# Kernel optimization log

Hardware: AMD Instinct MI355X
Metric: run time of the kernel (lower is better)

The kernel has to match this reference:

```python
import jax, jax.numpy as jnp
import numpy as np

B, N, E, H = 256, 256, 256, 512


def setup_inputs() -> dict:
    key = jax.random.key(0)
    ks = jax.random.split(key, 8)
    sH = 1.0 / np.sqrt(H)  # torch default init scale for LSTMCell / Linear fan_in
    sE = 1.0 / np.sqrt(E)
    return {
        "encoder_output": jax.random.normal(ks[0], (B, N, E), dtype=jnp.float32),
        "W_ih": jax.random.uniform(ks[1], (4 * H, E), jnp.float32, -sH, sH),
        "W_hh": jax.random.uniform(ks[2], (4 * H, H), jnp.float32, -sH, sH),
        "b_ih": jax.random.uniform(ks[3], (4 * H,), jnp.float32, -sH, sH),
        "b_hh": jax.random.uniform(ks[4], (4 * H,), jnp.float32, -sH, sH),
        "W_q": jax.random.uniform(ks[5], (H, H), jnp.float32, -sH, sH),
        "W_k": jax.random.uniform(ks[6], (H, E), jnp.float32, -sE, sE),
        "v": jax.random.uniform(ks[7], (H,), jnp.float32, -sH, sH),
        "max_steps": 256,
    }


def reference(encoder_output, W_ih, W_hh, b_ih, b_hh, W_q, W_k, v, max_steps):
    b, n, e = encoder_output.shape
    h_dim = W_hh.shape[1]
    # W_k(encoder_output) is loop-invariant -> hoist (same math as original)
    k_enc = jnp.einsum("bne,he->bnh", encoder_output, W_k)  # (B, N, H)
    keys = jax.random.split(jax.random.key(42), max_steps)
    batch_idx = jnp.arange(b)

    def step(carry, key):
        h, c, start, visited_mask = carry
        # torch LSTMCell: gates in i, f, g, o order
        gates = start @ W_ih.T + b_ih + h @ W_hh.T + b_hh  # (B, 4H)
        i, f, g, o = jnp.split(gates, 4, axis=-1)
        c = jax.nn.sigmoid(f) * c + jax.nn.sigmoid(i) * jnp.tanh(g)
        h = jax.nn.sigmoid(o) * jnp.tanh(c)
        q = h @ W_q.T  # (B, H)
        scores = jnp.einsum("bnh,h->bn", jnp.tanh(q[:, None, :] + k_enc), v)
        scores = scores - 1.0e6 * visited_mask
        probs = jax.nn.softmax(scores, axis=-1)
        # multinomial(probs, 1) == categorical over masked scores (logits)
        idx = jax.random.categorical(key, scores)  # (B,) int
        action_prob = jnp.take_along_axis(probs, idx[:, None], axis=1)[:, 0]
        visited_mask = visited_mask.at[batch_idx, idx].set(1.0)
        start = encoder_output[batch_idx, idx]  # (B, E)
        return (h, c, start, visited_mask), (idx, action_prob)

    init = (
        jnp.zeros((b, h_dim), jnp.float32),
        jnp.zeros((b, h_dim), jnp.float32),
        jnp.zeros((b, e), jnp.float32),
        jnp.zeros((b, n), jnp.float32),
    )
    _, (seq, action_probs) = jax.lax.scan(step, init, keys)
    action_sequence = seq.T  # (B, max_steps)
    logp_sum = jnp.sum(action_probs, axis=0)  # (B,) -- sums probs, as original does
    return action_sequence, logp_sum
```

## Files before the change

### kernel.cpp

```cpp
#include <hip/hip_runtime.h>
#include <cstdint>
#include <math.h>

typedef unsigned int u32;

#define BB 256
#define NN 256
#define EE 256
#define HH 512
#define G4 2048
#define KK 768
#define TT 256
#define NBLK 256
#define NTHR 1024

#define ALOADD(p)    __hip_atomic_load((p), __ATOMIC_RELAXED, __HIP_MEMORY_SCOPE_AGENT)
#define ASTORED(p,v) __hip_atomic_store((p), (v), __ATOMIC_RELAXED, __HIP_MEMORY_SCOPE_AGENT)
#define ALOADI(p)    __hip_atomic_load((p), __ATOMIC_RELAXED, __HIP_MEMORY_SCOPE_AGENT)
#define ASTOREI(p,v) __hip_atomic_store((p), (v), __ATOMIC_RELAXED, __HIP_MEMORY_SCOPE_AGENT)

__device__ __forceinline__ u32 rotl(u32 x, int d) { return (x << d) | (x >> (32 - d)); }

__device__ __forceinline__ void tf4(u32& x0, u32& x1, int r0, int r1, int r2, int r3) {
  x0 += x1; x1 = rotl(x1, r0); x1 ^= x0;
  x0 += x1; x1 = rotl(x1, r1); x1 ^= x0;
  x0 += x1; x1 = rotl(x1, r2); x1 ^= x0;
  x0 += x1; x1 = rotl(x1, r3); x1 ^= x0;
}

__device__ __forceinline__ void threefry2x32(u32 k0, u32 k1, u32 x0, u32 x1, u32& o0, u32& o1) {
  u32 k2 = k0 ^ k1 ^ 0x1BD11BDAu;
  x0 += k0; x1 += k1;
  tf4(x0, x1, 13, 15, 26, 6);  x0 += k1; x1 += k2 + 1u;
  tf4(x0, x1, 17, 29, 16, 24); x0 += k2; x1 += k0 + 2u;
  tf4(x0, x1, 13, 15, 26, 6);  x0 += k0; x1 += k1 + 3u;
  tf4(x0, x1, 17, 29, 16, 24); x0 += k1; x1 += k2 + 4u;
  tf4(x0, x1, 13, 15, 26, 6);  x0 += k2; x1 += k0 + 5u;
  o0 = x0; o1 = x1;
}

struct Args {
  const float *enc, *W_ih, *W_hh, *b_ih, *b_hh, *W_q, *W_k, *v;
  float *out;
  float *kT;
  float *Wc;
  float *WqT;
  double *bsum;
  u32 *keys;
  double *h0, *h1;
  double *c;
  double *q;
  int *idx;
  u32 *flags;
};

__device__ __forceinline__ void grid_barrier(u32* cnt, u32* gen) {
  __syncthreads();
  if (threadIdx.x == 0) {
    u32 g = __hip_atomic_load(gen, __ATOMIC_RELAXED, __HIP_MEMORY_SCOPE_AGENT);
    __threadfence();
    if (atomicAdd(cnt, 1u) == NBLK - 1u) {
      __hip_atomic_store(cnt, 0u, __ATOMIC_RELAXED, __HIP_MEMORY_SCOPE_AGENT);
      __threadfence();
      atomicAdd(gen, 1u);
    } else {
      while (__hip_atomic_load(gen, __ATOMIC_RELAXED, __HIP_MEMORY_SCOPE_AGENT) == g) {
        __builtin_amdgcn_s_sleep(2);
      }
    }
    __threadfence();
  }
  __syncthreads();
}

__device__ __forceinline__ void pod_signal(u32* ph, int pod, int me, u32 val) {
  asm volatile("s_waitcnt vmcnt(0)" ::: "memory");
  __syncthreads();
  if (threadIdx.x == 0) ASTOREI(&ph[pod * 32 + me], val);
}
__device__ __forceinline__ void pod_wait(u32* ph, int pod, u32 target) {
  const int t = threadIdx.x;
  if (t < 32) {
    while (ALOADI(&ph[pod * 32 + t]) < target) { __builtin_amdgcn_s_sleep(1); }
  }
  __syncthreads();
}

__global__ __launch_bounds__(NTHR) void mono_kernel(Args a) {
  const int blk = blockIdx.x;
  const int t = threadIdx.x;
  __shared__ alignas(16) unsigned char SMRAW[42368];
  __shared__ int visS[NN];
  __shared__ float vSp[HH];
  __shared__ double logpS;
  const int grp = blk >> 5;
  const int me  = blk & 31;
  const int jb = 4 * (blk & 7) + ((blk >> 3) & 3);
  u32* p1f = a.flags;
  u32* qf  = a.flags + 256;
  u32* p2f = a.flags + 512;

  {
    const int tid = blk * NTHR + t;
    const int tot = NBLK * NTHR;
    if (tid < BB * HH) { a.h0[tid] = 0.0; a.c[tid] = 0.0; }
    if (tid < BB) a.idx[tid] = -1;
    if (tid < 256) {
      u32 o0, o1;
      threefry2x32(0u, 42u, 0u, (u32)tid, o0, o1);
      a.keys[2 * tid] = o0; a.keys[2 * tid + 1] = o1;
    }
    if (tid < G4) a.bsum[tid] = (double)a.b_ih[tid] + (double)a.b_hh[tid];
    for (int i = tid; i < HH * HH; i += tot) {
      int h2 = i >> 9, h = i & 511;
      a.WqT[i] = a.W_q[h * HH + h2];
    }
    for (int i = tid; i < KK * G4; i += tot) {
      int k = i >> 11, col = i & 2047;
      int x16 = col >> 6, g = (col >> 4) & 3, w = col & 15;
      int j = g * HH + x16 * 16 + w;
      a.Wc[i] = (k < EE) ? a.W_ih[j * EE + k] : a.W_hh[j * HH + (k - EE)];
    }
    if (t < NN) visS[t] = 0;
    if (t < HH) vSp[t] = a.v[t];
    if (t == 0) logpS = 0.0;
  }
  {
    float (*encS)[65] = (float(*)[65])SMRAW;
    float (*wkS)[65]  = (float(*)[65])(SMRAW + 64 * 65 * 4);
    const int tn = t & 63, th = t >> 6;
    for (int tile = blk; tile < 8 * 4 * BB; tile += NBLK) {
      const int bx = tile & 7, by = (tile >> 3) & 3, b = tile >> 5;
      const int h0i = bx * 64, n0 = by * 64;
      double acc[4];
#pragma unroll
      for (int i = 0; i < 4; i++) acc[i] = 0.0;
      for (int ec = 0; ec < EE; ec += 64) {
        __syncthreads();
#pragma unroll
        for (int i = 0; i < 4; i++) {
          int idx = i * NTHR + t; int r = idx >> 6, cc = idx & 63;
          encS[r][cc] = a.enc[((size_t)b * NN + n0 + r) * EE + ec + cc];
          wkS[r][cc]  = a.W_k[(size_t)(h0i + r) * EE + ec + cc];
        }
        __syncthreads();
#pragma unroll 8
        for (int e = 0; e < 64; e++) {
          double ev = (double)encS[tn][e];
#pragma unroll
          for (int i = 0; i < 4; i++) acc[i] += (double)wkS[th * 4 + i][e] * ev;
        }
      }
#pragma unroll
      for (int i = 0; i < 4; i++)
        a.kT[((size_t)b * HH + h0i + th * 4 + i) * NN + n0 + tn] = (float)acc[i];
    }
  }
  grid_barrier(a.flags + 768, a.flags + 800);

  for (int step = 0; step < TT; step++) {
    double* hPrev = (step & 1) ? a.h1 : a.h0;
    double* hCur  = (step & 1) ? a.h0 : a.h1;
    const int b0 = grp * 32;

    if (step > 0) pod_wait(p2f, grp, (u32)step);

    {
      double (*aS)[33] = (double(*)[33])SMRAW;
      double (*bS)[66] = (double(*)[66])(SMRAW + 8448);
      int* idxP = (int*)(SMRAW + 25344);
      const int sr = t >> 5, scp = t & 31;
      const int bk = t >> 6, bc = t & 63;
      if (t < 32) idxP[t] = ALOADI(&a.idx[b0 + t]);
      __syncthreads();

      double aR; float bR0, bR1;
      {
        int iv = idxP[sr];
        aR = (iv >= 0) ? (double)a.enc[((size_t)(b0 + sr) * NN + iv) * EE + scp] : 0.0;
        bR0 = a.Wc[(size_t)(bk)      * G4 + jb * 64 + bc];
        bR1 = a.Wc[(size_t)(bk + 16) * G4 + jb * 64 + bc];
      }
      const int jc = t & 63, rg2 = t >> 6;
      double acc0, acc1, acc2, acc3;
      {
        double bv = a.bsum[(jc >> 4) * HH + jb * 16 + (jc & 15)];
        acc0 = bv; acc1 = bv; acc2 = bv; acc3 = bv;
      }
      for (int kc = 0; kc < KK; kc += 32) {
        aS[sr][scp] = aR;
        bS[bk][bc]      = (double)bR0;
        bS[bk + 16][bc] = (double)bR1;
        int kn = kc + 32;
        if (kn < KK) {
          if (kn < EE) {
            int iv = idxP[sr];
            aR = (iv >= 0) ? (double)a.enc[((size_t)(b0 + sr) * NN + iv) * EE + kn + scp] : 0.0;
          } else {
            aR = ALOADD(&hPrev[(size_t)(b0 + sr) * HH + (kn - EE) + scp]);
          }
          bR0 = a.Wc[(size_t)(kn + bk)      * G4 + jb * 64 + bc];
          bR1 = a.Wc[(size_t)(kn + bk + 16) * G4 + jb * 64 + bc];
        }
        __syncthreads();
        if (t < 512) {
#pragma unroll 8
          for (int kk = 0; kk < 32; kk++) {
            double bv = bS[kk][jc];
            acc0 += aS[rg2 * 4][kk]     * bv;
            acc1 += aS[rg2 * 4 + 1][kk] * bv;
            acc2 += aS[rg2 * 4 + 2][kk] * bv;
            acc3 += aS[rg2 * 4 + 3][kk] * bv;
          }
        }
        __syncthreads();
      }
      double (*gS)[66] = (double(*)[66])SMRAW;
      if (t < 512) {
        gS[rg2 * 4][jc]     = acc0;
        gS[rg2 * 4 + 1][jc] = acc1;
        gS[rg2 * 4 + 2][jc] = acc2;
        gS[rg2 * 4 + 3][jc] = acc3;
      }
      __syncthreads();
      if (t < 512) {
        const int b = t >> 4, w = t & 15;
        double ig = gS[b][w], fg = gS[b][16 + w], gv = gS[b][32 + w], og = gS[b][48 + w];
        double si = 1.0 / (1.0 + exp(-ig));
        double sf = 1.0 / (1.0 + exp(-fg));
        double so = 1.0 / (1.0 + exp(-og));
        size_t ci = (size_t)(b0 + b) * HH + jb * 16 + w;
        double cn = sf * a.c[ci] + si * tanh(gv);
        a.c[ci] = cn;
        ASTORED(&hCur[ci], so * tanh(cn));
      }
    }
    pod_signal(p1f, grp, me, (u32)(step + 1));
    pod_wait(p1f, grp, (u32)(step + 1));

    {
      double (*hS)[33] = (double(*)[33])SMRAW;
      float  (*wS)[17] = (float (*)[17])(SMRAW + 8448);
      const int sr = t >> 5, scp = t & 31;
      const int wk = t >> 4, wj = t & 15;
      const int j0 = jb * 16;
      double hR = ALOADD(&hCur[(size_t)(b0 + sr) * HH + scp]);
      float  wR = (t < 512) ? a.WqT[(size_t)wk * HH + j0 + wj] : 0.0f;
      const int bq = t >> 4, j = t & 15;
      double p0 = 0.0, p1 = 0.0, p2 = 0.0, p3 = 0.0;
      for (int kc = 0; kc < HH; kc += 32) {
        hS[sr][scp] = hR;
        if (t < 512) wS[wk][wj] = wR;
        int kn = kc + 32;
        if (kn < HH) {
          hR = ALOADD(&hCur[(size_t)(b0 + sr) * HH + kn + scp]);
          if (t < 512) wR = a.WqT[(size_t)(kn + wk) * HH + j0 + wj];
        }
        __syncthreads();
        if (t < 512) {
#pragma unroll 8
          for (int kk = 0; kk < 32; kk += 4) {
            p0 += hS[bq][kk]     * (double)wS[kk][j];
            p1 += hS[bq][kk + 1] * (double)wS[kk + 1][j];
            p2 += hS[bq][kk + 2] * (double)wS[kk + 2][j];
            p3 += hS[bq][kk + 3] * (double)wS[kk + 3][j];
          }
        }
        __syncthreads();
      }
      if (t < 512)
        ASTORED(&a.q[(size_t)(b0 + bq) * HH + j0 + j], (p0 + p1) + (p2 + p3));
    }
    pod_signal(qf, grp, me, (u32)(step + 1));
    pod_wait(qf, grp, (u32)(step + 1));

    {
      double* qS  = (double*)SMRAW;
      double* pS  = (double*)(SMRAW + 4096);
      double* sS  = (double*)(SMRAW + 37120);
      double* red = (double*)(SMRAW + 39168);
      int*   redi = (int*)(SMRAW + 41216);
      int*   idxS = (int*)(SMRAW + 42240);
      const int b = blk;
      if (t < 512) qS[t] = ALOADD(&a.q[(size_t)b * HH + t]);
      __syncthreads();

      const int col4 = (t & 63) * 4, slice = t >> 6;
      const float* kp = a.kT + ((size_t)b * HH + slice * 32) * NN + col4;
      double c0 = 0.0, c1 = 0.0, c2 = 0.0, c3 = 0.0;
#pragma unroll 4
      for (int h = 0; h < 32; h++) {
        float4 kv = *(const float4*)(kp + (size_t)h * NN);
        int hh = slice * 32 + h;
        double qh = qS[hh];
        double vh = (double)vSp[hh];
        c0 += vh * (double)tanhf((float)(qh + (double)kv.x));
        c1 += vh * (double)tanhf((float)(qh + (double)kv.y));
        c2 += vh * (double)tanhf((float)(qh + (double)kv.z));
        c3 += vh * (double)tanhf((float)(qh + (double)kv.w));
      }
      {
        double* pw = pS + slice * 258 + col4;
        pw[0] = c0; pw[1] = c1; pw[2] = c2; pw[3] = c3;
      }
      __syncthreads();

      if (t < 256) {
        double s = 0.0;
#pragma unroll
        for (int sl = 0; sl < 16; sl++) s += pS[sl * 258 + t];
        if (visS[t]) s -= 1.0e6;
        sS[t] = s;
      }
      __syncthreads();

      if (t < 256) {
        u32 fl = (u32)(b * 256 + t);
        u32 o0, o1;
        threefry2x32(a.keys[2 * step], a.keys[2 * step + 1], 0u, fl, o0, o1);
        u32 bits = o0 ^ o1;
        u32 fb = (bits >> 9) | 0x3F800000u;
        float uf = __uint_as_float(fb) - 1.0f;
        double uu = (uf > 0.0f) ? (double)uf : (double)1.17549435e-38f;
        double gmb = -log(-log(uu));
        red[t] = gmb + sS[t];
        redi[t] = t;
      }
      __syncthreads();
      for (int s2 = 128; s2 > 0; s2 >>= 1) {
        if (t < s2) {
          double v1 = red[t], v2 = red[t + s2];
          int i1 = redi[t], i2 = redi[t + s2];
          if (v2 > v1 || (v2 == v1 && i2 < i1)) { red[t] = v2; redi[t] = i2; }
        }
        __syncthreads();
      }
      if (t == 0) *idxS = redi[0];
      __syncthreads();

      if (t == 0) {
        int bi = *idxS;
        visS[bi] = 1;
        ASTOREI(&a.idx[b], bi);
      }
      pod_signal(p2f, grp, me, (u32)(step + 1));

      if (t < 256) red[t] = sS[t];
      __syncthreads();
      for (int s2 = 128; s2 > 0; s2 >>= 1) {
        if (t < s2) red[t] = fmax(red[t], red[t + s2]);
        __syncthreads();
      }
      double m = red[0];
      __syncthreads();
      if (t < 256) red[t] = exp(sS[t] - m);
      __syncthreads();
      for (int s2 = 128; s2 > 0; s2 >>= 1) {
        if (t < s2) red[t] += red[t + s2];
        __syncthreads();
      }
      if (t == 0) {
        int bi = *idxS;
        double p = exp(sS[bi] - m) / red[0];
        logpS += p;
        a.out[(size_t)b * TT + step] = (float)bi;
      }
      __syncthreads();
    }
  }

  if (t == 0) a.out[BB * TT + blk] = (float)logpS;
}

extern "C" void kernel_launch(void* const* d_in, const int* in_sizes, int n_in,
                              void* d_out, int out_size, void* d_ws, size_t ws_size,
                              hipStream_t stream) {
  char* ws = (char*)d_ws;
  Args a;
  a.enc  = (const float*)d_in[0];
  a.W_ih = (const float*)d_in[1];
  a.W_hh = (const float*)d_in[2];
  a.b_ih = (const float*)d_in[3];
  a.b_hh = (const float*)d_in[4];
  a.W_q  = (const float*)d_in[5];
  a.W_k  = (const float*)d_in[6];
  a.v    = (const float*)d_in[7];
  a.out  = (float*)d_out;

  a.kT    = (float*)(ws + 0);
  a.Wc    = (float*)(ws + 134217728);
  a.WqT   = (float*)(ws + 140509184);
  a.bsum  = (double*)(ws + 141557760);
  a.keys  = (u32*)(ws + 141574144);
  a.h0    = (double*)(ws + 141576192);
  a.h1    = (double*)(ws + 142624768);
  a.c     = (double*)(ws + 143673344);
  a.idx   = (int*)(ws + 144721920);
  a.flags = (u32*)(ws + 144723968);
  a.q     = (double*)(ws + 144728064);

  hipMemsetAsync((void*)a.flags, 0, 4096, stream);

  void* kargs[] = { &a };
  hipLaunchCooperativeKernel(reinterpret_cast<void*>(&mono_kernel),
                             dim3(NBLK), dim3(NTHR), kargs, 0, stream);
}
```

Baseline: 28.32 ms.

## Add 512-block x 512-thread cooperative kernel variant with occupancy-based dispatch

Adds a second persistent cooperative kernel that uses 512 blocks of 512 threads. Each pod of 32 blocks now handles 16 batch rows, and only half the blocks in each pod do the attention and sampling stage. Tile shapes for the k-precompute and gate GEMM are reshaped to fit the smaller blocks. A host-side occupancy query picks this variant when at least two blocks fit per CU and otherwise falls back to the original kernel. The aim is to use more CUs and shorten each per-step GEMM chain, in exchange for more flag traffic and idle blocks during the attention stage.

```diff
diff --git a/kernel.cpp b/kernel.cpp
--- a/kernel.cpp
+++ b/kernel.cpp
@@ -11,8 +11,6 @@
 #define G4 2048
 #define KK 768
 #define TT 256
-#define NBLK 256
-#define NTHR 1024
 
 #define ALOADD(p)    __hip_atomic_load((p), __ATOMIC_RELAXED, __HIP_MEMORY_SCOPE_AGENT)
 #define ASTORED(p,v) __hip_atomic_store((p), (v), __ATOMIC_RELAXED, __HIP_MEMORY_SCOPE_AGENT)
@@ -54,12 +52,12 @@
   u32 *flags;
 };
 
-__device__ __forceinline__ void grid_barrier(u32* cnt, u32* gen) {
+__device__ __forceinline__ void grid_barrier_n(u32* cnt, u32* gen, u32 nblk) {
   __syncthreads();
   if (threadIdx.x == 0) {
     u32 g = __hip_atomic_load(gen, __ATOMIC_RELAXED, __HIP_MEMORY_SCOPE_AGENT);
     __threadfence();
-    if (atomicAdd(cnt, 1u) == NBLK - 1u) {
+    if (atomicAdd(cnt, 1u) == nblk - 1u) {
       __hip_atomic_store(cnt, 0u, __ATOMIC_RELAXED, __HIP_MEMORY_SCOPE_AGENT);
       __threadfence();
       atomicAdd(gen, 1u);
@@ -78,15 +76,320 @@
   __syncthreads();
   if (threadIdx.x == 0) ASTOREI(&ph[pod * 32 + me], val);
 }
-__device__ __forceinline__ void pod_wait(u32* ph, int pod, u32 target) {
+__device__ __forceinline__ void pod_wait(u32* ph, int pod, int nsig, u32 target) {
   const int t = threadIdx.x;
-  if (t < 32) {
+  if (t < nsig) {
     while (ALOADI(&ph[pod * 32 + t]) < target) { __builtin_amdgcn_s_sleep(1); }
   }
   __syncthreads();
 }
 
-__global__ __launch_bounds__(NTHR) void mono_kernel(Args a) {
+__global__ __launch_bounds__(512, 4) void mono512_kernel(Args a) {
+  const int blk = blockIdx.x;
+  const int t = threadIdx.x;
+  __shared__ alignas(16) unsigned char SMRAW[25792];
+  __shared__ int visS[NN];
+  __shared__ float vSp[HH];
+  __shared__ double logpS;
+  const int grp = blk >> 5;
+  const int me  = blk & 31;
+  const int jb = 4 * (blk & 7) + ((blk >> 3) & 3);
+  u32* p1f = a.flags;
+  u32* qf  = a.flags + 512;
+  u32* p2f = a.flags + 1024;
+
+  {
+    const int tid = blk * 512 + t;
+    const int tot = 512 * 512;
+    if (tid < BB * HH) { a.h0[tid] = 0.0; a.c[tid] = 0.0; }
+    if (tid < BB) a.idx[tid] = -1;
+    if (tid < 256) {
+      u32 o0, o1;
+      threefry2x32(0u, 42u, 0u, (u32)tid, o0, o1);
+      a.keys[2 * tid] = o0; a.keys[2 * tid + 1] = o1;
+    }
+    if (tid < G4) a.bsum[tid] = (double)a.b_ih[tid] + (double)a.b_hh[tid];
+    for (int i = tid; i < HH * HH; i += tot) {
+      int h2 = i >> 9, h = i & 511;
+      a.WqT[i] = a.W_q[h * HH + h2];
+    }
+    for (int i = tid; i < KK * G4; i += tot) {
+      int k = i >> 11, col = i & 2047;
+      int x16 = col >> 6, g = (col >> 4) & 3, w = col & 15;
+      int j = g * HH + x16 * 16 + w;
+      a.Wc[i] = (k < EE) ? a.W_ih[j * EE + k] : a.W_hh[j * HH + (k - EE)];
+    }
+    if (t < NN) visS[t] = 0;
+    if (t < HH) vSp[t] = a.v[t];
+    if (t == 0) logpS = 0.0;
+  }
+  {
+    float (*encS)[33] = (float(*)[33])SMRAW;
+    float (*wkS)[33]  = (float(*)[33])(SMRAW + 8448);
+    const int tn = t & 63, th = t >> 6;
+    for (int tile = blk; tile < 8 * 4 * BB; tile += 512) {
+      const int bx = tile & 7, by = (tile >> 3) & 3, b = tile >> 5;
+      const int h0i = bx * 64, n0 = by * 64;
+      double acc[8];
+#pragma unroll
+      for (int i = 0; i < 8; i++) acc[i] = 0.0;
+      for (int ec = 0; ec < EE; ec += 32) {
+        __syncthreads();
+#pragma unroll
+        for (int i = 0; i < 4; i++) {
+          int idx = i * 512 + t; int r = idx >> 5, cc = idx & 31;
+          encS[r][cc] = a.enc[((size_t)b * NN + n0 + r) * EE + ec + cc];
+          wkS[r][cc]  = a.W_k[(size_t)(h0i + r) * EE + ec + cc];
+        }
+        __syncthreads();
+#pragma unroll 8
+        for (int e = 0; e < 32; e++) {
+          double ev = (double)encS[tn][e];
+#pragma unroll
+          for (int i = 0; i < 8; i++) acc[i] += (double)wkS[th * 8 + i][e] * ev;
+        }
+      }
+#pragma unroll
+      for (int i = 0; i < 8; i++)
+        a.kT[((size_t)b * HH + h0i + th * 8 + i) * NN + n0 + tn] = (float)acc[i];
+    }
+  }
+  grid_barrier_n(a.flags + 1536, a.flags + 1568, 512u);
+
+  for (int step = 0; step < TT; step++) {
+    double* hPrev = (step & 1) ? a.h1 : a.h0;
+    double* hCur  = (step & 1) ? a.h0 : a.h1;
+    const int b0 = grp * 16;
+
+    if (step > 0) pod_wait(p2f, grp, 16, (u32)step);
+
+    {
+      double (*aS)[33] = (double(*)[33])SMRAW;
+      double (*bS)[66] = (double(*)[66])(SMRAW + 4224);
+      int* idxP = (int*)(SMRAW + 21120);
+      const int sr = t >> 5, scp = t & 31;
+      const int bk = t >> 6, bc = t & 63;
+      if (t < 16) idxP[t] = ALOADI(&a.idx[b0 + t]);
+      __syncthreads();
+
+      double aR; float bR0, bR1, bR2, bR3;
+      {
+        int iv = idxP[sr];
+        aR = (iv >= 0) ? (double)a.enc[((size_t)(b0 + sr) * NN + iv) * EE + scp] : 0.0;
+        bR0 = a.Wc[(size_t)(bk)      * G4 + jb * 64 + bc];
+        bR1 = a.Wc[(size_t)(bk + 8)  * G4 + jb * 64 + bc];
+        bR2 = a.Wc[(size_t)(bk + 16) * G4 + jb * 64 + bc];
+        bR3 = a.Wc[(size_t)(bk + 24) * G4 + jb * 64 + bc];
+      }
+      const int jc = t & 63, rg2 = t >> 6;
+      double acc0, acc1;
+      {
+        double bv = a.bsum[(jc >> 4) * HH + jb * 16 + (jc & 15)];
+        acc0 = bv; acc1 = bv;
+      }
+      for (int kc = 0; kc < KK; kc += 32) {
+        aS[sr][scp] = aR;
+        bS[bk][bc]      = (double)bR0;
+        bS[bk + 8][bc]  = (double)bR1;
+        bS[bk + 16][bc] = (double)bR2;
+        bS[bk + 24][bc] = (double)bR3;
+        int kn = kc + 32;
+        if (kn < KK) {
+          if (kn < EE) {
+            int iv = idxP[sr];
+            aR = (iv >= 0) ? (double)a.enc[((size_t)(b0 + sr) * NN + iv) * EE + kn + scp] : 0.0;
+          } else {
+            aR = ALOADD(&hPrev[(size_t)(b0 + sr) * HH + (kn - EE) + scp]);
+          }
+          bR0 = a.Wc[(size_t)(kn + bk)      * G4 + jb * 64 + bc];
+          bR1 = a.Wc[(size_t)(kn + bk + 8)  * G4 + jb * 64 + bc];
+          bR2 = a.Wc[(size_t)(kn + bk + 16) * G4 + jb * 64 + bc];
+          bR3 = a.Wc[(size_t)(kn + bk + 24) * G4 + jb * 64 + bc];
+        }
+        __syncthreads();
+#pragma unroll 8
+        for (int kk = 0; kk < 32; kk++) {
+          double bv = bS[kk][jc];
+          acc0 += aS[rg2 * 2][kk]     * bv;
+          acc1 += aS[rg2 * 2 + 1][kk] * bv;
+        }
+        __syncthreads();
+      }
+      double (*gS)[66] = (double(*)[66])SMRAW;
+      gS[rg2 * 2][jc]     = acc0;
+      gS[rg2 * 2 + 1][jc] = acc1;
+      __syncthreads();
+      if (t < 256) {
+        const int b = t >> 4, w = t & 15;
+        double ig = gS[b][w], fg = gS[b][16 + w], gv = gS[b][32 + w], og = gS[b][48 + w];
+        double si = 1.0 / (1.0 + exp(-ig));
+        double sf = 1.0 / (1.0 + exp(-fg));
+        double so = 1.0 / (1.0 + exp(-og));
+        size_t ci = (size_t)(b0 + b) * HH + jb * 16 + w;
+        double cn = sf * a.c[ci] + si * tanh(gv);
+        a.c[ci] = cn;
+        ASTORED(&hCur[ci], so * tanh(cn));
+      }
+    }
+    pod_signal(p1f, grp, me, (u32)(step + 1));
+    pod_wait(p1f, grp, 32, (u32)(step + 1));
+
+    {
+      double (*hS)[33] = (double(*)[33])SMRAW;
+      float  (*wS)[17] = (float (*)[17])(SMRAW + 4224);
+      const int sr = t >> 5, scp = t & 31;
+      const int wk = t >> 4, wj = t & 15;
+      const int j0 = jb * 16;
+      double hR = ALOADD(&hCur[(size_t)(b0 + sr) * HH + scp]);
+      float  wR = a.WqT[(size_t)wk * HH + j0 + wj];
+      const int bq = t >> 4, j = t & 15;
+      double p0 = 0.0, p1 = 0.0, p2 = 0.0, p3 = 0.0;
+      for (int kc = 0; kc < HH; kc += 32) {
+        hS[sr][scp] = hR;
+        wS[wk][wj] = wR;
+        int kn = kc + 32;
+        if (kn < HH) {
+          hR = ALOADD(&hCur[(size_t)(b0 + sr) * HH + kn + scp]);
+          wR = a.WqT[(size_t)(kn + wk) * HH + j0 + wj];
+        }
+        __syncthreads();
+        if (t < 256) {
+#pragma unroll 8
+          for (int kk = 0; kk < 32; kk += 4) {
+            p0 += hS[bq][kk]     * (double)wS[kk][j];
+            p1 += hS[bq][kk + 1] * (double)wS[kk + 1][j];
+            p2 += hS[bq][kk + 2] * (double)wS[kk + 2][j];
+            p3 += hS[bq][kk + 3] * (double)wS[kk + 3][j];
+          }
+        }
+        __syncthreads();
+      }
+      if (t < 256)
+        ASTORED(&a.q[(size_t)(b0 + bq) * HH + j0 + j], (p0 + p1) + (p2 + p3));
+    }
+    pod_signal(qf, grp, me, (u32)(step + 1));
+    pod_wait(qf, grp, 32, (u32)(step + 1));
+
+    if (me < 16) {
+      double* qS  = (double*)SMRAW;
+      double* pS  = (double*)(SMRAW + 4096);
+      double* sS  = (double*)(SMRAW + 20608);
+      double* red = (double*)(SMRAW + 22656);
+      int*   redi = (int*)(SMRAW + 24704);
+      int*   idxS = (int*)(SMRAW + 25728);
+      const int b = b0 + me;
+      qS[t] = ALOADD(&a.q[(size_t)b * HH + t]);
+      __syncthreads();
+
+      const int col4 = (t & 63) * 4, slice0 = t >> 6;
+      double m0, m1, m2, m3;
+      {
+        const float* kp = a.kT + ((size_t)b * HH + slice0 * 32) * NN + col4;
+        double c0 = 0.0, c1 = 0.0, c2 = 0.0, c3 = 0.0;
+#pragma unroll 4
+        for (int h = 0; h < 32; h++) {
+          float4 kv = *(const float4*)(kp + (size_t)h * NN);
+          int hh = slice0 * 32 + h;
+          double qh = qS[hh];
+          double vh = (double)vSp[hh];
+          c0 += vh * (double)tanhf((float)(qh + (double)kv.x));
+          c1 += vh * (double)tanhf((float)(qh + (double)kv.y));
+          c2 += vh * (double)tanhf((float)(qh + (double)kv.z));
+          c3 += vh * (double)tanhf((float)(qh + (double)kv.w));
+        }
+        m0 = c0; m1 = c1; m2 = c2; m3 = c3;
+      }
+      {
+        const int slice = slice0 + 8;
+        const float* kp = a.kT + ((size_t)b * HH + slice * 32) * NN + col4;
+        double c0 = 0.0, c1 = 0.0, c2 = 0.0, c3 = 0.0;
+#pragma unroll 4
+        for (int h = 0; h < 32; h++) {
+          float4 kv = *(const float4*)(kp + (size_t)h * NN);
+          int hh = slice * 32 + h;
+          double qh = qS[hh];
+          double vh = (double)vSp[hh];
+          c0 += vh * (double)tanhf((float)(qh + (double)kv.x));
+          c1 += vh * (double)tanhf((float)(qh + (double)kv.y));
+          c2 += vh * (double)tanhf((float)(qh + (double)kv.z));
+          c3 += vh * (double)tanhf((float)(qh + (double)kv.w));
+        }
+        m0 += c0; m1 += c1; m2 += c2; m3 += c3;
+      }
+      {
+        double* pw = pS + slice0 * 258 + col4;
+        pw[0] = m0; pw[1] = m1; pw[2] = m2; pw[3] = m3;
+      }
+      __syncthreads();
+
+      if (t < 256) {
+        double s = 0.0;
+#pragma unroll
+        for (int sl = 0; sl < 8; sl++) s += pS[sl * 258 + t];
+        if (visS[t]) s -= 1.0e6;
+        sS[t] = s;
+      }
+      __syncthreads();
+
+      if (t < 256) {
+        u32 fl = (u32)(b * 256 + t);
+        u32 o0, o1;
+        threefry2x32(a.keys[2 * step], a.keys[2 * step + 1], 0u, fl, o0, o1);
+        u32 bits = o0 ^ o1;
+        u32 fb = (bits >> 9) | 0x3F800000u;
+        float uf = __uint_as_float(fb) - 1.0f;
+        double uu = (uf > 0.0f) ? (double)uf : (double)1.17549435e-38f;
+        double gmb = -log(-log(uu));
+        red[t] = gmb + sS[t];
+        redi[t] = t;
+      }
+      __syncthreads();
+      for (int s2 = 128; s2 > 0; s2 >>= 1) {
+        if (t < s2) {
+          double v1 = red[t], v2 = red[t + s2];
+          int i1 = redi[t], i2 = redi[t + s2];
+          if (v2 > v1 || (v2 == v1 && i2 < i1)) { red[t] = v2; redi[t] = i2; }
+        }
+        __syncthreads();
+      }
+      if (t == 0) *idxS = redi[0];
+      __syncthreads();
+
+      if (t == 0) {
+        int bi = *idxS;
+        visS[bi] = 1;
+        ASTOREI(&a.idx[b], bi);
+      }
+      pod_signal(p2f, grp, me, (u32)(step + 1));
+
+      if (t < 256) red[t] = sS[t];
+      __syncthreads();
+      for (int s2 = 128; s2 > 0; s2 >>= 1) {
+        if (t < s2) red[t] = fmax(red[t], red[t + s2]);
+        __syncthreads();
+      }
+      double m = red[0];
+      __syncthreads();
+      if (t < 256) red[t] = exp(sS[t] - m);
+      __syncthreads();
+      for (int s2 = 128; s2 > 0; s2 >>= 1) {
+        if (t < s2) red[t] += red[t + s2];
+        __syncthreads();
+      }
+      if (t == 0) {
+        int bi = *idxS;
+        double p = exp(sS[bi] - m) / red[0];
+        logpS += p;
+        a.out[(size_t)b * TT + step] = (float)bi;
+      }
+      __syncthreads();
+    }
+  }
+
+  if (me < 16 && t == 0) a.out[BB * TT + (grp * 16 + me)] = (float)logpS;
+}
+
+__global__ __launch_bounds__(1024) void mono1024_kernel(Args a) {
   const int blk = blockIdx.x;
   const int t = threadIdx.x;
   __shared__ alignas(16) unsigned char SMRAW[42368];
@@ -101,8 +404,8 @@
   u32* p2f = a.flags + 512;
 
   {
-    const int tid = blk * NTHR + t;
-    const int tot = NBLK * NTHR;
+    const int tid = blk * 1024 + t;
+    const int tot = 256 * 1024;
     if (tid < BB * HH) { a.h0[tid] = 0.0; a.c[tid] = 0.0; }
     if (tid < BB) a.idx[tid] = -1;
     if (tid < 256) {
@@ -129,7 +432,7 @@
     float (*encS)[65] = (float(*)[65])SMRAW;
     float (*wkS)[65]  = (float(*)[65])(SMRAW + 64 * 65 * 4);
     const int tn = t & 63, th = t >> 6;
-    for (int tile = blk; tile < 8 * 4 * BB; tile += NBLK) {
+    for (int tile = blk; tile < 8 * 4 * BB; tile += 256) {
       const int bx = tile & 7, by = (tile >> 3) & 3, b = tile >> 5;
       const int h0i = bx * 64, n0 = by * 64;
       double acc[4];
@@ -139,7 +442,7 @@
         __syncthreads();
 #pragma unroll
         for (int i = 0; i < 4; i++) {
-          int idx = i * NTHR + t; int r = idx >> 6, cc = idx & 63;
+          int idx = i * 1024 + t; int r = idx >> 6, cc = idx & 63;
           encS[r][cc] = a.enc[((size_t)b * NN + n0 + r) * EE + ec + cc];
           wkS[r][cc]  = a.W_k[(size_t)(h0i + r) * EE + ec + cc];
         }
@@ -156,14 +459,14 @@
         a.kT[((size_t)b * HH + h0i + th * 4 + i) * NN + n0 + tn] = (float)acc[i];
     }
   }
-  grid_barrier(a.flags + 768, a.flags + 800);
+  grid_barrier_n(a.flags + 768, a.flags + 800, 256u);
 
   for (int step = 0; step < TT; step++) {
     double* hPrev = (step & 1) ? a.h1 : a.h0;
     double* hCur  = (step & 1) ? a.h0 : a.h1;
     const int b0 = grp * 32;
 
-    if (step > 0) pod_wait(p2f, grp, (u32)step);
+    if (step > 0) pod_wait(p2f, grp, 32, (u32)step);
 
     {
       double (*aS)[33] = (double(*)[33])SMRAW;
@@ -236,7 +539,7 @@
       }
     }
     pod_signal(p1f, grp, me, (u32)(step + 1));
-    pod_wait(p1f, grp, (u32)(step + 1));
+    pod_wait(p1f, grp, 32, (u32)(step + 1));
 
     {
       double (*hS)[33] = (double(*)[33])SMRAW;
@@ -272,7 +575,7 @@
         ASTORED(&a.q[(size_t)(b0 + bq) * HH + j0 + j], (p0 + p1) + (p2 + p3));
     }
     pod_signal(qf, grp, me, (u32)(step + 1));
-    pod_wait(qf, grp, (u32)(step + 1));
+    pod_wait(qf, grp, 32, (u32)(step + 1));
 
     {
       double* qS  = (double*)SMRAW;
@@ -397,11 +700,19 @@
   a.c     = (double*)(ws + 143673344);
   a.idx   = (int*)(ws + 144721920);
   a.flags = (u32*)(ws + 144723968);
-  a.q     = (double*)(ws + 144728064);
-
-  hipMemsetAsync((void*)a.flags, 0, 4096, stream);
-
+  a.q     = (double*)(ws + 144732160);
+
+  hipMemsetAsync((void*)a.flags, 0, 8192, stream);
+
+  int occ = 0;
+  hipError_t qe = hipOccupancyMaxActiveBlocksPerMultiprocessor(
+      &occ, reinterpret_cast<const void*>(mono512_kernel), 512, 0);
   void* kargs[] = { &a };
-  hipLaunchCooperativeKernel(reinterpret_cast<void*>(&mono_kernel),
-                             dim3(NBLK), dim3(NTHR), kargs, 0, stream);
+  if (qe == hipSuccess && occ >= 2) {
+    hipLaunchCooperativeKernel(reinterpret_cast<void*>(&mono512_kernel),
+                               dim3(512), dim3(512), kargs, 0, stream);
+  } else {
+    hipLaunchCooperativeKernel(reinterpret_cast<void*>(&mono1024_kernel),
+                               dim3(256), dim3(1024), kargs, 0, stream);
+  }
 }
```

After: 28.34 ms. No clear change (+0.1%).

## Repartition LSTM step into 4-block pods of 4 batch rows

Applied to the files above, without the earlier changes.

Per-step work moves from 32-block pods covering 32 batch rows each to 4-block pods covering 4 batch rows each. Each block now computes 512 gate columns (a quarter of all gates) and 128 query columns, streaming weights straight from global memory instead of staging tiles in shared memory. The aim is to shrink the inter-block synchronisation scope per step to 4 blocks. The cost is roughly eight times more weight traffic per step, because weights are reused across only 4 batch rows instead of 32, and the 6 MB Wc matrix does not fit in L2.

```diff
diff --git a/kernel.cpp b/kernel.cpp
--- a/kernel.cpp
+++ b/kernel.cpp
@@ -54,12 +54,12 @@
   u32 *flags;
 };
 
-__device__ __forceinline__ void grid_barrier(u32* cnt, u32* gen) {
+__device__ __forceinline__ void grid_barrier_n(u32* cnt, u32* gen, u32 nblk) {
   __syncthreads();
   if (threadIdx.x == 0) {
     u32 g = __hip_atomic_load(gen, __ATOMIC_RELAXED, __HIP_MEMORY_SCOPE_AGENT);
     __threadfence();
-    if (atomicAdd(cnt, 1u) == NBLK - 1u) {
+    if (atomicAdd(cnt, 1u) == nblk - 1u) {
       __hip_atomic_store(cnt, 0u, __ATOMIC_RELAXED, __HIP_MEMORY_SCOPE_AGENT);
       __threadfence();
       atomicAdd(gen, 1u);
@@ -76,12 +76,12 @@
 __device__ __forceinline__ void pod_signal(u32* ph, int pod, int me, u32 val) {
   asm volatile("s_waitcnt vmcnt(0)" ::: "memory");
   __syncthreads();
-  if (threadIdx.x == 0) ASTOREI(&ph[pod * 32 + me], val);
+  if (threadIdx.x == 0) ASTOREI(&ph[pod * 4 + me], val);
 }
 __device__ __forceinline__ void pod_wait(u32* ph, int pod, u32 target) {
   const int t = threadIdx.x;
-  if (t < 32) {
-    while (ALOADI(&ph[pod * 32 + t]) < target) { __builtin_amdgcn_s_sleep(1); }
+  if (t < 4) {
+    while (ALOADI(&ph[pod * 4 + t]) < target) { __builtin_amdgcn_s_sleep(1); }
   }
   __syncthreads();
 }
@@ -93,9 +93,9 @@
   __shared__ int visS[NN];
   __shared__ float vSp[HH];
   __shared__ double logpS;
-  const int grp = blk >> 5;
-  const int me  = blk & 31;
-  const int jb = 4 * (blk & 7) + ((blk >> 3) & 3);
+  const int pod = blk >> 2;
+  const int me  = blk & 3;
+  const int b0  = pod * 4;
   u32* p1f = a.flags;
   u32* qf  = a.flags + 256;
   u32* p2f = a.flags + 512;
@@ -116,9 +116,9 @@
       a.WqT[i] = a.W_q[h * HH + h2];
     }
     for (int i = tid; i < KK * G4; i += tot) {
-      int k = i >> 11, col = i & 2047;
-      int x16 = col >> 6, g = (col >> 4) & 3, w = col & 15;
-      int j = g * HH + x16 * 16 + w;
+      int k = i >> 11, colp = i & 2047;
+      int mb = colp >> 9, g = (colp >> 7) & 3, w = colp & 127;
+      int j = g * 512 + mb * 128 + w;
       a.Wc[i] = (k < EE) ? a.W_ih[j * EE + k] : a.W_hh[j * HH + (k - EE)];
     }
     if (t < NN) visS[t] = 0;
@@ -156,123 +156,93 @@
         a.kT[((size_t)b * HH + h0i + th * 4 + i) * NN + n0 + tn] = (float)acc[i];
     }
   }
-  grid_barrier(a.flags + 768, a.flags + 800);
+  grid_barrier_n(a.flags + 768, a.flags + 800, (u32)NBLK);
 
   for (int step = 0; step < TT; step++) {
     double* hPrev = (step & 1) ? a.h1 : a.h0;
     double* hCur  = (step & 1) ? a.h0 : a.h1;
-    const int b0 = grp * 32;
-
-    if (step > 0) pod_wait(p2f, grp, (u32)step);
+
+    if (step > 0) pod_wait(p2f, pod, (u32)step);
 
     {
       double (*aS)[33] = (double(*)[33])SMRAW;
-      double (*bS)[66] = (double(*)[66])(SMRAW + 8448);
-      int* idxP = (int*)(SMRAW + 25344);
-      const int sr = t >> 5, scp = t & 31;
-      const int bk = t >> 6, bc = t & 63;
-      if (t < 32) idxP[t] = ALOADI(&a.idx[b0 + t]);
-      __syncthreads();
-
-      double aR; float bR0, bR1;
-      {
-        int iv = idxP[sr];
-        aR = (iv >= 0) ? (double)a.enc[((size_t)(b0 + sr) * NN + iv) * EE + scp] : 0.0;
-        bR0 = a.Wc[(size_t)(bk)      * G4 + jb * 64 + bc];
-        bR1 = a.Wc[(size_t)(bk + 16) * G4 + jb * 64 + bc];
-      }
-      const int jc = t & 63, rg2 = t >> 6;
-      double acc0, acc1, acc2, acc3;
-      {
-        double bv = a.bsum[(jc >> 4) * HH + jb * 16 + (jc & 15)];
+      int* idxP = (int*)(SMRAW + 1056);
+      double (*gS)[512] = (double(*)[512])(SMRAW + 2048);
+      if (t < 4) idxP[t] = ALOADI(&a.idx[b0 + t]);
+      __syncthreads();
+
+      double acc0 = 0.0, acc1 = 0.0, acc2 = 0.0, acc3 = 0.0;
+      if (t < 512) {
+        int g = t >> 7, w = t & 127;
+        double bv = a.bsum[g * 512 + me * 128 + w];
         acc0 = bv; acc1 = bv; acc2 = bv; acc3 = bv;
       }
       for (int kc = 0; kc < KK; kc += 32) {
-        aS[sr][scp] = aR;
-        bS[bk][bc]      = (double)bR0;
-        bS[bk + 16][bc] = (double)bR1;
-        int kn = kc + 32;
-        if (kn < KK) {
-          if (kn < EE) {
-            int iv = idxP[sr];
-            aR = (iv >= 0) ? (double)a.enc[((size_t)(b0 + sr) * NN + iv) * EE + kn + scp] : 0.0;
+        if (t < 128) {
+          int b = t >> 5, kk = t & 31;
+          double v;
+          if (kc < EE) {
+            int iv = idxP[b];
+            v = (iv >= 0) ? (double)a.enc[((size_t)(b0 + b) * NN + iv) * EE + kc + kk] : 0.0;
           } else {
-            aR = ALOADD(&hPrev[(size_t)(b0 + sr) * HH + (kn - EE) + scp]);
+            v = ALOADD(&hPrev[(size_t)(b0 + b) * HH + (kc - EE) + kk]);
           }
-          bR0 = a.Wc[(size_t)(kn + bk)      * G4 + jb * 64 + bc];
-          bR1 = a.Wc[(size_t)(kn + bk + 16) * G4 + jb * 64 + bc];
+          aS[b][kk] = v;
         }
         __syncthreads();
         if (t < 512) {
+          const float* wp = &a.Wc[(size_t)kc * G4 + me * 512 + t];
 #pragma unroll 8
           for (int kk = 0; kk < 32; kk++) {
-            double bv = bS[kk][jc];
-            acc0 += aS[rg2 * 4][kk]     * bv;
-            acc1 += aS[rg2 * 4 + 1][kk] * bv;
-            acc2 += aS[rg2 * 4 + 2][kk] * bv;
-            acc3 += aS[rg2 * 4 + 3][kk] * bv;
+            double bd = (double)wp[(size_t)kk * G4];
+            acc0 += aS[0][kk] * bd;
+            acc1 += aS[1][kk] * bd;
+            acc2 += aS[2][kk] * bd;
+            acc3 += aS[3][kk] * bd;
           }
         }
         __syncthreads();
       }
-      double (*gS)[66] = (double(*)[66])SMRAW;
       if (t < 512) {
-        gS[rg2 * 4][jc]     = acc0;
-        gS[rg2 * 4 + 1][jc] = acc1;
-        gS[rg2 * 4 + 2][jc] = acc2;
-        gS[rg2 * 4 + 3][jc] = acc3;
+        gS[0][t] = acc0; gS[1][t] = acc1; gS[2][t] = acc2; gS[3][t] = acc3;
       }
       __syncthreads();
       if (t < 512) {
-        const int b = t >> 4, w = t & 15;
-        double ig = gS[b][w], fg = gS[b][16 + w], gv = gS[b][32 + w], og = gS[b][48 + w];
+        const int b = t >> 7, w = t & 127;
+        double ig = gS[b][w], fg = gS[b][128 + w], gv = gS[b][256 + w], og = gS[b][384 + w];
         double si = 1.0 / (1.0 + exp(-ig));
         double sf = 1.0 / (1.0 + exp(-fg));
         double so = 1.0 / (1.0 + exp(-og));
-        size_t ci = (size_t)(b0 + b) * HH + jb * 16 + w;
+        size_t ci = (size_t)(b0 + b) * HH + me * 128 + w;
         double cn = sf * a.c[ci] + si * tanh(gv);
         a.c[ci] = cn;
         ASTORED(&hCur[ci], so * tanh(cn));
       }
     }
-    pod_signal(p1f, grp, me, (u32)(step + 1));
-    pod_wait(p1f, grp, (u32)(step + 1));
+    pod_signal(p1f, pod, me, (u32)(step + 1));
+    pod_wait(p1f, pod, (u32)(step + 1));
 
     {
-      double (*hS)[33] = (double(*)[33])SMRAW;
-      float  (*wS)[17] = (float (*)[17])(SMRAW + 8448);
-      const int sr = t >> 5, scp = t & 31;
-      const int wk = t >> 4, wj = t & 15;
-      const int j0 = jb * 16;
-      double hR = ALOADD(&hCur[(size_t)(b0 + sr) * HH + scp]);
-      float  wR = (t < 512) ? a.WqT[(size_t)wk * HH + j0 + wj] : 0.0f;
-      const int bq = t >> 4, j = t & 15;
-      double p0 = 0.0, p1 = 0.0, p2 = 0.0, p3 = 0.0;
-      for (int kc = 0; kc < HH; kc += 32) {
-        hS[sr][scp] = hR;
-        if (t < 512) wS[wk][wj] = wR;
-        int kn = kc + 32;
-        if (kn < HH) {
-          hR = ALOADD(&hCur[(size_t)(b0 + sr) * HH + kn + scp]);
-          if (t < 512) wR = a.WqT[(size_t)(kn + wk) * HH + j0 + wj];
-        }
-        __syncthreads();
-        if (t < 512) {
+      double (*hS)[512] = (double(*)[512])SMRAW;
+      for (int i = t; i < 4 * HH; i += NTHR)
+        hS[i >> 9][i & 511] = ALOADD(&hCur[(size_t)(b0 + (i >> 9)) * HH + (i & 511)]);
+      __syncthreads();
+      if (t < 512) {
+        const int b = t >> 7, jl = t & 127, j = me * 128 + jl;
+        const float* wp = a.WqT + j;
+        double p0 = 0.0, p1 = 0.0, p2 = 0.0, p3 = 0.0;
 #pragma unroll 8
-          for (int kk = 0; kk < 32; kk += 4) {
-            p0 += hS[bq][kk]     * (double)wS[kk][j];
-            p1 += hS[bq][kk + 1] * (double)wS[kk + 1][j];
-            p2 += hS[bq][kk + 2] * (double)wS[kk + 2][j];
-            p3 += hS[bq][kk + 3] * (double)wS[kk + 3][j];
-          }
-        }
-        __syncthreads();
-      }
-      if (t < 512)
-        ASTORED(&a.q[(size_t)(b0 + bq) * HH + j0 + j], (p0 + p1) + (p2 + p3));
-    }
-    pod_signal(qf, grp, me, (u32)(step + 1));
-    pod_wait(qf, grp, (u32)(step + 1));
+        for (int k = 0; k < HH; k += 4) {
+          p0 += hS[b][k]     * (double)wp[(size_t)k * HH];
+          p1 += hS[b][k + 1] * (double)wp[(size_t)(k + 1) * HH];
+          p2 += hS[b][k + 2] * (double)wp[(size_t)(k + 2) * HH];
+          p3 += hS[b][k + 3] * (double)wp[(size_t)(k + 3) * HH];
+        }
+        ASTORED(&a.q[(size_t)(b0 + b) * HH + j], (p0 + p1) + (p2 + p3));
+      }
+    }
+    pod_signal(qf, pod, me, (u32)(step + 1));
+    pod_wait(qf, pod, (u32)(step + 1));
 
     {
       double* qS  = (double*)SMRAW;
@@ -343,7 +313,7 @@
         visS[bi] = 1;
         ASTOREI(&a.idx[b], bi);
       }
-      pod_signal(p2f, grp, me, (u32)(step + 1));
+      pod_signal(p2f, pod, me, (u32)(step + 1));
 
       if (t < 256) red[t] = sS[t];
       __syncthreads();
```

Result: slower. 95.70 ms (+237.9%).
